# Optimization experiments

Hardware: AMD Instinct MI355X
Metric: run time of the kernel (lower is better)

Reference implementation:

```python
import jax, jax.numpy as jnp
import numpy as np

ATT_HEAD = 12
IN_DIM = 768
OUT_DIM = IN_DIM // ATT_HEAD
LEAKY_ALPHA = 0.2
B, N = 8, 512


def setup_inputs() -> dict:
    key = jax.random.key(0)
    ks = jax.random.split(key, 8)
    feat_in = jax.random.normal(ks[0], (B, N, IN_DIM), dtype=jnp.float32)
    adj = jax.random.randint(ks[1], (B, N, N), 0, 2) > 0
    # xavier_uniform for W: fan_in=in_dim, fan_out=out_dim
    lim_W = float(np.sqrt(6.0 / (IN_DIM + OUT_DIM)))
    W = jax.random.uniform(ks[2], (ATT_HEAD, IN_DIM, OUT_DIM), minval=-lim_W, maxval=lim_W, dtype=jnp.float32)
    b = jnp.zeros((OUT_DIM,), dtype=jnp.float32)
    lim_w = float(np.sqrt(6.0 / (OUT_DIM + 1)))
    w_src = jax.random.uniform(ks[3], (ATT_HEAD, OUT_DIM, 1), minval=-lim_w, maxval=lim_w, dtype=jnp.float32)
    w_dst = jax.random.uniform(ks[4], (ATT_HEAD, OUT_DIM, 1), minval=-lim_w, maxval=lim_w, dtype=jnp.float32)
    # xavier_normal for H.weight [in_dim, in_dim]
    std_H = float(np.sqrt(2.0 / (IN_DIM + IN_DIM)))
    H_w = jax.random.normal(ks[5], (IN_DIM, IN_DIM), dtype=jnp.float32) * std_H
    H_b = jax.random.normal(ks[6], (IN_DIM,), dtype=jnp.float32) * 0.01
    return {"feat_in": feat_in, "adj": adj, "W": W, "b": b,
            "w_src": w_src, "w_dst": w_dst, "H_w": H_w, "H_b": H_b}


def reference(feat_in, adj, W, b, w_src, w_dst, H_w, H_b):
    # h: [B, heads, N, out_dim]
    h = jnp.einsum('bnd,ade->bane', feat_in, W)
    th = jnp.tanh(h)
    attn_src = jnp.einsum('bane,aeo->bano', th, w_src)  # [B,A,N,1]
    attn_dst = jnp.einsum('bane,aeo->bano', th, w_dst)  # [B,A,N,1]
    attn = attn_src + jnp.swapaxes(attn_dst, 2, 3)      # [B,A,N,N]
    attn = jnp.where(attn >= 0, attn, LEAKY_ALPHA * attn)
    mask = ~adj[:, None, :, :]                           # [B,1,N,N]
    attn = jnp.where(mask, jnp.float32(-999.0), attn)
    attn = jax.nn.softmax(attn, axis=-1)
    feat_out = jnp.einsum('banm,bame->bane', attn, h) + b
    feat_out = jnp.swapaxes(feat_out, 1, 2).reshape(feat_in.shape[0], feat_in.shape[1], -1)
    feat_out = jax.nn.elu(feat_out)
    gate = jax.nn.sigmoid(feat_in @ H_w.T + H_b)
    return gate * feat_out + (1.0 - gate) * feat_in
```

## Files before the change

kernel.cpp:

```cpp
#include <hip/hip_runtime.h>
#include <hip/hip_bf16.h>

#define BB 8
#define NN 512
#define AH 12
#define DIN 768
#define EE 64
#define MM (BB*NN)
#define YY (BB*AH)
#define LEAKY 0.2f

typedef unsigned short u16;
typedef unsigned int u32;
typedef __attribute__((ext_vector_type(8))) short short8;
typedef __attribute__((ext_vector_type(4))) float f32x4;
typedef __attribute__((ext_vector_type(4))) u32 u32x4;

static __device__ __forceinline__ u16 f2bf(float f) {
    u32 u = __builtin_bit_cast(u32, f);
    u32 r = (u + 0x7FFFu + ((u >> 16) & 1u)) >> 16;
    return (u16)r;
}
static __device__ __forceinline__ u32 pk2(float a, float b) {
    return (u32)f2bf(a) | ((u32)f2bf(b) << 16);
}
static __device__ __forceinline__ u32 pk2t(float a, float b) {
    return (__builtin_bit_cast(u32, a) >> 16) | (__builtin_bit_cast(u32, b) & 0xFFFF0000u);
}
static __device__ __forceinline__ float ftanh(float x) {
    x = fminf(fmaxf(x, -15.f), 15.f);
    return 1.f - 2.f / (__expf(2.f * x) + 1.f);
}
static __device__ __forceinline__ void gl_lds16(const u16* g, u16* l) {
    __builtin_amdgcn_global_load_lds((const __attribute__((address_space(1))) unsigned int*)g,
                                     (__attribute__((address_space(3))) unsigned int*)l,
                                     16, 0, 0);
}

static __device__ __forceinline__ void mfma_probe(int lane, int* prow, int* pcol) {
    int q = lane >> 4, x = lane & 15;
    short8 af, bf;
#pragma unroll
    for (int j = 0; j < 8; j++) {
        int k = q * 8 + j;
        af[j] = (short)f2bf((k < 16) ? (float)(x * 16 + k) : 0.f);
        bf[j] = (short)f2bf((k == x) ? 1.f : 0.f);
    }
    f32x4 d = {};
    d = __builtin_amdgcn_mfma_f32_16x16x32_bf16(af, bf, d, 0, 0, 0);
#pragma unroll
    for (int r = 0; r < 4; r++) {
        int v = (int)(d[r] + 0.5f);
        prow[r] = v >> 4;
        pcol[r] = v & 15;
    }
}

#define N_FEAT (MM*DIN)
#define N_W    (AH*DIN*EE)
#define PACK_BLOCKS (MM/4)
#define CONV_BLOCKS ((N_FEAT + 2*N_W)/256)
__global__ __launch_bounds__(256) void prep_kernel(const int* __restrict__ adj,
                                                   const float* __restrict__ feat,
                                                   const float* __restrict__ W,
                                                   const float* __restrict__ Hw,
                                                   u32* __restrict__ maskbuf,
                                                   u16* __restrict__ featb,
                                                   u16* __restrict__ Wt,
                                                   u16* __restrict__ Hwb) {
    int blk = blockIdx.x, t = threadIdx.x;
    if (blk < PACK_BLOCKS) {
        int w = t >> 6, ln = t & 63;
        int row = blk * 4 + w;
        const int* ar = adj + (size_t)row * NN;
#pragma unroll
        for (int it = 0; it < 8; it++) {
            unsigned long long bal = __ballot(ar[it * 64 + ln] != 0);
            if (ln == 0) {
                maskbuf[row * 16 + it * 2]     = (u32)bal;
                maskbuf[row * 16 + it * 2 + 1] = (u32)(bal >> 32);
            }
        }
        return;
    }
    int i = (blk - PACK_BLOCKS) * 256 + t;
    if (i < N_FEAT) { featb[i] = f2bf(feat[i]); return; }
    int i2 = i - N_FEAT;
    if (i2 < N_W) {
        int a = i2 / (DIN * EE), rem = i2 % (DIN * EE);
        int e = rem / DIN, d = rem % DIN;
        Wt[i2] = f2bf(W[a * (DIN * EE) + d * EE + e]);
        return;
    }
    int i3 = i2 - N_W;
    Hwb[i3] = f2bf(Hw[i3]);
}

#define GEMM_CORE(Abase, Bbase)                                               \
    int wm = w & 1, wn = w >> 1, xr = x & 7;                                  \
    int srow = t >> 3;                                                        \
    int skoff = ((t & 7) ^ (srow & 7)) * 8;                                   \
    const u16* Agp = (Abase) + srow * DIN + skoff;                            \
    const u16* Bgp = (Bbase) + srow * DIN + skoff;                            \
    u16* Asw = As + w * 512;                                                  \
    u16* Bsw = Bs + w * 512;                                                  \
    const u16* ApA = As + (wm * 32 + x) * 64;                                 \
    const u16* ApB = Bs + (wn * 32 + x) * 64;                                 \
    f32x4 acc00 = {}, acc01 = {}, acc10 = {}, acc11 = {};                     \
    for (int k0 = 0; k0 < DIN; k0 += 64) {                                    \
        gl_lds16(Agp + k0, Asw);                                              \
        gl_lds16(Agp + 32 * DIN + k0, Asw + 2048);                            \
        gl_lds16(Bgp + k0, Bsw);                                              \
        gl_lds16(Bgp + 32 * DIN + k0, Bsw + 2048);                            \
        __syncthreads();                                                      \
        _Pragma("unroll")                                                     \
        for (int kk = 0; kk < 2; kk++) {                                      \
            int c8 = ((q + kk * 4) ^ xr) * 8;                                 \
            short8 a0 = *(const short8*)(ApA + c8);                           \
            short8 a1 = *(const short8*)(ApA + 16 * 64 + c8);                 \
            short8 b0 = *(const short8*)(ApB + c8);                           \
            short8 b1 = *(const short8*)(ApB + 16 * 64 + c8);                 \
            acc00 = __builtin_amdgcn_mfma_f32_16x16x32_bf16(a0, b0, acc00, 0, 0, 0); \
            acc01 = __builtin_amdgcn_mfma_f32_16x16x32_bf16(a0, b1, acc01, 0, 0, 0); \
            acc10 = __builtin_amdgcn_mfma_f32_16x16x32_bf16(a1, b0, acc10, 0, 0, 0); \
            acc11 = __builtin_amdgcn_mfma_f32_16x16x32_bf16(a1, b1, acc11, 0, 0, 0); \
        }                                                                     \
        __syncthreads();                                                      \
    }                                                                         \
    int prow[4], pcol[4];                                                     \
    mfma_probe(lane, prow, pcol);                                             \
    _Pragma("unroll")                                                         \
    for (int r = 0; r < 4; r++) {                                             \
        cs[wm * 32 + prow[r]][wn * 32 + pcol[r]]           = acc00[r];        \
        cs[wm * 32 + prow[r]][wn * 32 + 16 + pcol[r]]      = acc01[r];        \
        cs[wm * 32 + 16 + prow[r]][wn * 32 + pcol[r]]      = acc10[r];        \
        cs[wm * 32 + 16 + prow[r]][wn * 32 + 16 + pcol[r]] = acc11[r];        \
    }                                                                         \
    __syncthreads();

static __device__ __forceinline__ float sigm(float z) {
    z = fminf(fmaxf(z, -80.f), 80.f);
    return 1.f / (1.f + __expf(-z));
}

__global__ __launch_bounds__(256) void gemm_fused_kernel(const u16* __restrict__ featb,
                                                         const u16* __restrict__ Wt,
                                                         const u16* __restrict__ Hwb,
                                                         const float* __restrict__ wsrc,
                                                         const float* __restrict__ wdst,
                                                         const float* __restrict__ Hb,
                                                         u16* __restrict__ hT,
                                                         float2* __restrict__ Spair,
                                                         float2* __restrict__ Dpair,
                                                         float* __restrict__ Gbuf) {
    __shared__ u16 As[64 * 64];
    __shared__ u16 Bs[64 * 64];
    __shared__ alignas(16) float cs[64][68];
    int t = threadIdx.x, w = t >> 6, lane = t & 63, q = lane >> 4, x = lane & 15;
    int m0 = blockIdx.x * 64;
    int yb = blockIdx.y;

    if (yb < AH) {
        int a = yb;
        GEMM_CORE(featb + (size_t)m0 * DIN, Wt + (size_t)a * EE * DIN)

        int b = m0 >> 9;
        int y = b * AH + a;
        int nbase = m0 & 511;
        {
            int e = t >> 2, ng = t & 3;
            u32* dst = (u32*)&hT[((size_t)y * EE + e) * NN + nbase + ng * 16];
#pragma unroll
            for (int i = 0; i < 8; i++)
                dst[i] = pk2(cs[ng * 16 + 2 * i][e], cs[ng * 16 + 2 * i + 1][e]);
        }
        {
            int r = t >> 2, cg = t & 3;
            float s = 0.f, d = 0.f;
#pragma unroll
            for (int i = 0; i < 16; i++) {
                int e2 = cg * 16 + i;
                float th = ftanh(cs[r][e2]);
                s += th * wsrc[a * EE + e2];
                d += th * wdst[a * EE + e2];
            }
            s += __shfl_xor(s, 1); s += __shfl_xor(s, 2);
            d += __shfl_xor(d, 1); d += __shfl_xor(d, 2);
            if (cg == 0) {
                s = fminf(fmaxf(s, -40.f), 40.f);
                d = fminf(fmaxf(d, -40.f), 40.f);
                Spair[y * NN + nbase + r] = make_float2(__expf(s), __expf(0.2f * s));
                Dpair[y * NN + nbase + r] = make_float2(__expf(d), __expf(0.2f * d));
            }
        }
    } else {
        int n0 = (yb - AH) * 64;
        GEMM_CORE(featb + (size_t)m0 * DIN, Hwb + (size_t)n0 * DIN)

        float4 hb = *(const float4*)&Hb[n0 + (t & 15) * 4];
#pragma unroll
        for (int p = 0; p < 4; p++) {
            int ml = p * 16 + (t >> 4), c4 = (t & 15) * 4;
            float4 v4 = *(const float4*)&cs[ml][c4];
            size_t idx = (size_t)(m0 + ml) * DIN + n0 + c4;
            float4 o;
            o.x = sigm(v4.x + hb.x);
            o.y = sigm(v4.y + hb.y);
            o.z = sigm(v4.z + hb.z);
            o.w = sigm(v4.w + hb.w);
            *(float4*)&Gbuf[idx] = o;
        }
    }
}

__global__ __launch_bounds__(256) void attn_kernel(const u16* __restrict__ hT,
                                                   const float2* __restrict__ Spair,
                                                   const float2* __restrict__ Dpair,
                                                   const u32* __restrict__ maskbuf,
                                                   const float* __restrict__ bias,
                                                   const float* __restrict__ Gbuf,
                                                   const float* __restrict__ feat,
                                                   float* __restrict__ out) {
    __shared__ alignas(16) float2 sd2[NN];
    __shared__ u32 smask[64][17];
    __shared__ float silv[64];
    __shared__ alignas(16) float cs[64][68];

    int t = threadIdx.x;
    int y = blockIdx.y, bb = y / AH, a = y % AH;
    int i0 = blockIdx.x * 64;

    sd2[t] = Dpair[y * NN + t];
    sd2[t + 256] = Dpair[y * NN + 256 + t];
#pragma unroll
    for (int p = 0; p < 4; p++) {
        int idx = p * 256 + t, r = idx >> 4, c = idx & 15;
        smask[r][c] = maskbuf[((bb << 9) + i0 + r) * 16 + c];
    }
    __syncthreads();

    int w = t >> 6, lane = t & 63, q = lane >> 4, x = lane & 15;
    int rowl = w * 16 + x;
    float2 se = Spair[y * NN + i0 + rowl];
    float es1 = se.x, es2 = se.y;

    u32 anym = 0;
#pragma unroll
    for (int c = 0; c < 16; c++) anym |= smask[rowl][c];
    int uni = (anym == 0);

    const u16* hTy = hT + (size_t)y * EE * NN;
    f32x4 acc[4] = {};
    float lsum = 0.f;

#pragma unroll 2
    for (int k0 = 0; k0 < NN; k0 += 32) {
        u32 mb = smask[rowl][k0 >> 5] >> (q * 8);
        float pv[8];
#pragma unroll
        for (int j = 0; j < 8; j++) {
            float2 dp = sd2[k0 + q * 8 + j];
            float m1 = es1 * dp.x;
            float m2 = es2 * dp.y;
            float p = (m1 >= 1.f) ? m1 : m2;
            p = ((mb >> j) & 1) ? p : 0.f;
            p = uni ? 1.0f : p;
            lsum += p;
            pv[j] = p;
        }
        short8 af = __builtin_bit_cast(short8, (u32x4){
            pk2t(pv[0], pv[1]), pk2t(pv[2], pv[3]),
            pk2t(pv[4], pv[5]), pk2t(pv[6], pv[7])});
        const u16* hp = hTy + (size_t)x * NN + k0 + q * 8;
        short8 b0 = *(const short8*)(hp);
        short8 b1 = *(const short8*)(hp + 16 * NN);
        short8 b2 = *(const short8*)(hp + 32 * NN);
        short8 b3 = *(const short8*)(hp + 48 * NN);
        acc[0] = __builtin_amdgcn_mfma_f32_16x16x32_bf16(af, b0, acc[0], 0, 0, 0);
        acc[1] = __builtin_amdgcn_mfma_f32_16x16x32_bf16(af, b1, acc[1], 0, 0, 0);
        acc[2] = __builtin_amdgcn_mfma_f32_16x16x32_bf16(af, b2, acc[2], 0, 0, 0);
        acc[3] = __builtin_amdgcn_mfma_f32_16x16x32_bf16(af, b3, acc[3], 0, 0, 0);
    }

    lsum += __shfl_xor(lsum, 16);
    lsum += __shfl_xor(lsum, 32);
    if (q == 0) silv[rowl] = 1.f / fmaxf(lsum, 1e-30f);

    int prow[4], pcol[4];
    mfma_probe(lane, prow, pcol);
#pragma unroll
    for (int nt = 0; nt < 4; nt++)
#pragma unroll
        for (int r = 0; r < 4; r++)
            cs[w * 16 + prow[r]][nt * 16 + pcol[r]] = acc[nt][r];
    __syncthreads();

    float4 b4 = *(const float4*)&bias[(t & 15) * 4];
#pragma unroll
    for (int p = 0; p < 4; p++) {
        int nl = p * 16 + (t >> 4), e4 = (t & 15) * 4;
        float il = silv[nl];
        float4 c4 = *(const float4*)&cs[nl][e4];
        size_t base = ((size_t)(bb << 9) + i0 + nl) * DIN + a * EE + e4;
        float4 g4 = *(const float4*)&Gbuf[base];
        float4 f4 = *(const float4*)&feat[base];
        float4 o;
        float v, e;
        v = c4.x * il + b4.x; e = v > 0.f ? v : __expf(v) - 1.f; o.x = g4.x * e + (1.f - g4.x) * f4.x;
        v = c4.y * il + b4.y; e = v > 0.f ? v : __expf(v) - 1.f; o.y = g4.y * e + (1.f - g4.y) * f4.y;
        v = c4.z * il + b4.z; e = v > 0.f ? v : __expf(v) - 1.f; o.z = g4.z * e + (1.f - g4.z) * f4.z;
        v = c4.w * il + b4.w; e = v > 0.f ? v : __expf(v) - 1.f; o.w = g4.w * e + (1.f - g4.w) * f4.w;
        *(float4*)&out[base] = o;
    }
}

extern "C" void kernel_launch(void* const* d_in, const int* in_sizes, int n_in,
                              void* d_out, int out_size, void* d_ws, size_t ws_size,
                              hipStream_t stream) {
    const float* feat  = (const float*)d_in[0];
    const int*   adj   = (const int*)  d_in[1];
    const float* W     = (const float*)d_in[2];
    const float* bvec  = (const float*)d_in[3];
    const float* wsrc  = (const float*)d_in[4];
    const float* wdst  = (const float*)d_in[5];
    const float* Hw    = (const float*)d_in[6];
    const float* Hb    = (const float*)d_in[7];
    float* out = (float*)d_out;

    char* ws = (char*)d_ws;
    u16*    featb   = (u16*)(ws);
    u16*    Wt      = (u16*)(ws + 6291456);
    u16*    Hwb     = (u16*)(ws + 7471104);
    u16*    hT      = (u16*)(ws + 8650752);
    float2* Spair   = (float2*)(ws + 14942208);
    float2* Dpair   = (float2*)(ws + 15335424);
    u32*    maskbuf = (u32*)(ws + 15728640);
    float*  Gbuf    = (float*)(ws + 15990784);

    prep_kernel<<<PACK_BLOCKS + CONV_BLOCKS, 256, 0, stream>>>(
        adj, feat, W, Hw, maskbuf, featb, Wt, Hwb);
    gemm_fused_kernel<<<dim3(MM / 64, 2 * AH), 256, 0, stream>>>(
        featb, Wt, Hwb, wsrc, wdst, Hb, hT, Spair, Dpair, Gbuf);
    attn_kernel<<<dim3(NN / 64, YY), 256, 0, stream>>>(
        hT, Spair, Dpair, maskbuf, bvec, Gbuf, feat, out);
}
```

Before: 137.4 us.

## Move gate GEMM into attention kernel to eliminate Gbuf round trip

Moves the sigmoid gate GEMM (feat @ H_w^T) out of the first GEMM kernel and into the attention kernel. Each attention block now computes its own 64x64 gate tile in registers, with the GEMM staging buffers sharing LDS with the mask and Dpair arrays through a union. This removes the 12.6MB fp32 Gbuf write and read and halves the first GEMM's grid. In exchange, the attention kernel becomes longer and uses more registers, and the gate GEMM now runs serially before the attention work inside each block.

```diff
diff --git a/kernel.cpp b/kernel.cpp
--- a/kernel.cpp
+++ b/kernel.cpp
@@ -30,6 +30,10 @@
 static __device__ __forceinline__ float ftanh(float x) {
     x = fminf(fmaxf(x, -15.f), 15.f);
     return 1.f - 2.f / (__expf(2.f * x) + 1.f);
+}
+static __device__ __forceinline__ float sigm(float z) {
+    z = fminf(fmaxf(z, -80.f), 80.f);
+    return 1.f / (1.f + __expf(-z));
 }
 static __device__ __forceinline__ void gl_lds16(const u16* g, u16* l) {
     __builtin_amdgcn_global_load_lds((const __attribute__((address_space(1))) unsigned int*)g,
@@ -138,77 +142,48 @@
     }                                                                         \
     __syncthreads();
 
-static __device__ __forceinline__ float sigm(float z) {
-    z = fminf(fmaxf(z, -80.f), 80.f);
-    return 1.f / (1.f + __expf(-z));
-}
-
-__global__ __launch_bounds__(256) void gemm_fused_kernel(const u16* __restrict__ featb,
-                                                         const u16* __restrict__ Wt,
-                                                         const u16* __restrict__ Hwb,
-                                                         const float* __restrict__ wsrc,
-                                                         const float* __restrict__ wdst,
-                                                         const float* __restrict__ Hb,
-                                                         u16* __restrict__ hT,
-                                                         float2* __restrict__ Spair,
-                                                         float2* __restrict__ Dpair,
-                                                         float* __restrict__ Gbuf) {
+__global__ __launch_bounds__(256) void gemm_h_kernel(const u16* __restrict__ featb,
+                                                     const u16* __restrict__ Wt,
+                                                     const float* __restrict__ wsrc,
+                                                     const float* __restrict__ wdst,
+                                                     u16* __restrict__ hT,
+                                                     float2* __restrict__ Spair,
+                                                     float2* __restrict__ Dpair) {
     __shared__ u16 As[64 * 64];
     __shared__ u16 Bs[64 * 64];
     __shared__ alignas(16) float cs[64][68];
     int t = threadIdx.x, w = t >> 6, lane = t & 63, q = lane >> 4, x = lane & 15;
-    int m0 = blockIdx.x * 64;
-    int yb = blockIdx.y;
-
-    if (yb < AH) {
-        int a = yb;
-        GEMM_CORE(featb + (size_t)m0 * DIN, Wt + (size_t)a * EE * DIN)
-
-        int b = m0 >> 9;
-        int y = b * AH + a;
-        int nbase = m0 & 511;
-        {
-            int e = t >> 2, ng = t & 3;
-            u32* dst = (u32*)&hT[((size_t)y * EE + e) * NN + nbase + ng * 16];
-#pragma unroll
-            for (int i = 0; i < 8; i++)
-                dst[i] = pk2(cs[ng * 16 + 2 * i][e], cs[ng * 16 + 2 * i + 1][e]);
-        }
-        {
-            int r = t >> 2, cg = t & 3;
-            float s = 0.f, d = 0.f;
-#pragma unroll
-            for (int i = 0; i < 16; i++) {
-                int e2 = cg * 16 + i;
-                float th = ftanh(cs[r][e2]);
-                s += th * wsrc[a * EE + e2];
-                d += th * wdst[a * EE + e2];
-            }
-            s += __shfl_xor(s, 1); s += __shfl_xor(s, 2);
-            d += __shfl_xor(d, 1); d += __shfl_xor(d, 2);
-            if (cg == 0) {
-                s = fminf(fmaxf(s, -40.f), 40.f);
-                d = fminf(fmaxf(d, -40.f), 40.f);
-                Spair[y * NN + nbase + r] = make_float2(__expf(s), __expf(0.2f * s));
-                Dpair[y * NN + nbase + r] = make_float2(__expf(d), __expf(0.2f * d));
-            }
-        }
-    } else {
-        int n0 = (yb - AH) * 64;
-        GEMM_CORE(featb + (size_t)m0 * DIN, Hwb + (size_t)n0 * DIN)
-
-        float4 hb = *(const float4*)&Hb[n0 + (t & 15) * 4];
-#pragma unroll
-        for (int p = 0; p < 4; p++) {
-            int ml = p * 16 + (t >> 4), c4 = (t & 15) * 4;
-            float4 v4 = *(const float4*)&cs[ml][c4];
-            size_t idx = (size_t)(m0 + ml) * DIN + n0 + c4;
-            float4 o;
-            o.x = sigm(v4.x + hb.x);
-            o.y = sigm(v4.y + hb.y);
-            o.z = sigm(v4.z + hb.z);
-            o.w = sigm(v4.w + hb.w);
-            *(float4*)&Gbuf[idx] = o;
+    int m0 = blockIdx.x * 64, a = blockIdx.y;
+
+    GEMM_CORE(featb + (size_t)m0 * DIN, Wt + (size_t)a * EE * DIN)
+
+    int b = m0 >> 9;
+    int y = b * AH + a;
+    int nbase = m0 & 511;
+    {
+        int e = t >> 2, ng = t & 3;
+        u32* dst = (u32*)&hT[((size_t)y * EE + e) * NN + nbase + ng * 16];
+#pragma unroll
+        for (int i = 0; i < 8; i++)
+            dst[i] = pk2(cs[ng * 16 + 2 * i][e], cs[ng * 16 + 2 * i + 1][e]);
+    }
+    {
+        int r = t >> 2, cg = t & 3;
+        float s = 0.f, d = 0.f;
+#pragma unroll
+        for (int i = 0; i < 16; i++) {
+            int e2 = cg * 16 + i;
+            float th = ftanh(cs[r][e2]);
+            s += th * wsrc[a * EE + e2];
+            d += th * wdst[a * EE + e2];
+        }
+        s += __shfl_xor(s, 1); s += __shfl_xor(s, 2);
+        d += __shfl_xor(d, 1); d += __shfl_xor(d, 2);
+        if (cg == 0) {
+            s = fminf(fmaxf(s, -40.f), 40.f);
+            d = fminf(fmaxf(d, -40.f), 40.f);
+            Spair[y * NN + nbase + r] = make_float2(__expf(s), __expf(0.2f * s));
+            Dpair[y * NN + nbase + r] = make_float2(__expf(d), __expf(0.2f * d));
         }
     }
 }
@@ -218,18 +193,45 @@
                                                    const float2* __restrict__ Dpair,
                                                    const u32* __restrict__ maskbuf,
                                                    const float* __restrict__ bias,
-                                                   const float* __restrict__ Gbuf,
+                                                   const u16* __restrict__ featb,
+                                                   const u16* __restrict__ Hwb,
+                                                   const float* __restrict__ Hb,
                                                    const float* __restrict__ feat,
                                                    float* __restrict__ out) {
-    __shared__ alignas(16) float2 sd2[NN];
-    __shared__ u32 smask[64][17];
+    __shared__ union {
+        u16 stage[2][64 * 64];
+        struct {
+            float2 sd2[NN];
+            u32 smask[64][17];
+        } pv;
+    } ushr;
+    __shared__ alignas(16) float cs[64][68];
     __shared__ float silv[64];
-    __shared__ alignas(16) float cs[64][68];
 
     int t = threadIdx.x;
     int y = blockIdx.y, bb = y / AH, a = y % AH;
     int i0 = blockIdx.x * 64;
-
+    int w = t >> 6, lane = t & 63, q = lane >> 4, x = lane & 15;
+
+    float4 g4[4];
+    {
+        u16* As = ushr.stage[0];
+        u16* Bs = ushr.stage[1];
+        GEMM_CORE(featb + ((size_t)(bb << 9) + i0) * DIN, Hwb + (size_t)(a * EE) * DIN)
+        float4 hb = *(const float4*)&Hb[a * EE + (t & 15) * 4];
+#pragma unroll
+        for (int p = 0; p < 4; p++) {
+            int ml = p * 16 + (t >> 4), c4 = (t & 15) * 4;
+            float4 v4 = *(const float4*)&cs[ml][c4];
+            g4[p].x = sigm(v4.x + hb.x);
+            g4[p].y = sigm(v4.y + hb.y);
+            g4[p].z = sigm(v4.z + hb.z);
+            g4[p].w = sigm(v4.w + hb.w);
+        }
+    }
+
+    float2* sd2 = ushr.pv.sd2;
+    u32 (*smask)[17] = ushr.pv.smask;
     sd2[t] = Dpair[y * NN + t];
     sd2[t + 256] = Dpair[y * NN + 256 + t];
 #pragma unroll
@@ -239,7 +241,6 @@
     }
     __syncthreads();
 
-    int w = t >> 6, lane = t & 63, q = lane >> 4, x = lane & 15;
     int rowl = w * 16 + x;
     float2 se = Spair[y * NN + i0 + rowl];
     float es1 = se.x, es2 = se.y;
@@ -302,14 +303,14 @@
         float il = silv[nl];
         float4 c4 = *(const float4*)&cs[nl][e4];
         size_t base = ((size_t)(bb << 9) + i0 + nl) * DIN + a * EE + e4;
-        float4 g4 = *(const float4*)&Gbuf[base];
         float4 f4 = *(const float4*)&feat[base];
+        float4 g = g4[p];
         float4 o;
         float v, e;
-        v = c4.x * il + b4.x; e = v > 0.f ? v : __expf(v) - 1.f; o.x = g4.x * e + (1.f - g4.x) * f4.x;
-        v = c4.y * il + b4.y; e = v > 0.f ? v : __expf(v) - 1.f; o.y = g4.y * e + (1.f - g4.y) * f4.y;
-        v = c4.z * il + b4.z; e = v > 0.f ? v : __expf(v) - 1.f; o.z = g4.z * e + (1.f - g4.z) * f4.z;
-        v = c4.w * il + b4.w; e = v > 0.f ? v : __expf(v) - 1.f; o.w = g4.w * e + (1.f - g4.w) * f4.w;
+        v = c4.x * il + b4.x; e = v > 0.f ? v : __expf(v) - 1.f; o.x = g.x * e + (1.f - g.x) * f4.x;
+        v = c4.y * il + b4.y; e = v > 0.f ? v : __expf(v) - 1.f; o.y = g.y * e + (1.f - g.y) * f4.y;
+        v = c4.z * il + b4.z; e = v > 0.f ? v : __expf(v) - 1.f; o.z = g.z * e + (1.f - g.z) * f4.z;
+        v = c4.w * il + b4.w; e = v > 0.f ? v : __expf(v) - 1.f; o.w = g.w * e + (1.f - g.w) * f4.w;
         *(float4*)&out[base] = o;
     }
 }
@@ -335,12 +336,11 @@
     float2* Spair   = (float2*)(ws + 14942208);
     float2* Dpair   = (float2*)(ws + 15335424);
     u32*    maskbuf = (u32*)(ws + 15728640);
-    float*  Gbuf    = (float*)(ws + 15990784);
 
     prep_kernel<<<PACK_BLOCKS + CONV_BLOCKS, 256, 0, stream>>>(
         adj, feat, W, Hw, maskbuf, featb, Wt, Hwb);
-    gemm_fused_kernel<<<dim3(MM / 64, 2 * AH), 256, 0, stream>>>(
-        featb, Wt, Hwb, wsrc, wdst, Hb, hT, Spair, Dpair, Gbuf);
+    gemm_h_kernel<<<dim3(MM / 64, AH), 256, 0, stream>>>(
+        featb, Wt, wsrc, wdst, hT, Spair, Dpair);
     attn_kernel<<<dim3(NN / 64, YY), 256, 0, stream>>>(
-        hT, Spair, Dpair, maskbuf, bvec, Gbuf, feat, out);
-}
+        hT, Spair, Dpair, maskbuf, bvec, featb, Hwb, Hb, feat, out);
+}
```

Result: no change. 136.1 us (-0.9%).

## Merge W and gate GEMM blocks sharing feature tile; block hT layout

Applied to the files above, without the earlier changes.

Each GEMM block now computes both the per-head projection and the matching 64-column slice of the gate GEMM, so the feature tile is loaded into LDS once for both. The grid's y dimension shrinks from 2*AH to AH. hT is also re-laid out in 8-element k-chunks so that the attention kernel's B-operand loads become contiguous 16-byte vectors across lanes rather than strided rows. In exchange each block uses more LDS and accumulator registers and there are half as many blocks, which can lower occupancy.

```diff
diff --git a/kernel.cpp b/kernel.cpp
--- a/kernel.cpp
+++ b/kernel.cpp
@@ -30,6 +30,10 @@
 static __device__ __forceinline__ float ftanh(float x) {
     x = fminf(fmaxf(x, -15.f), 15.f);
     return 1.f - 2.f / (__expf(2.f * x) + 1.f);
+}
+static __device__ __forceinline__ float sigm(float z) {
+    z = fminf(fmaxf(z, -80.f), 80.f);
+    return 1.f / (1.f + __expf(-z));
 }
 static __device__ __forceinline__ void gl_lds16(const u16* g, u16* l) {
     __builtin_amdgcn_global_load_lds((const __attribute__((address_space(1))) unsigned int*)g,
@@ -96,53 +100,6 @@
     Hwb[i3] = f2bf(Hw[i3]);
 }
 
-#define GEMM_CORE(Abase, Bbase)                                               \
-    int wm = w & 1, wn = w >> 1, xr = x & 7;                                  \
-    int srow = t >> 3;                                                        \
-    int skoff = ((t & 7) ^ (srow & 7)) * 8;                                   \
-    const u16* Agp = (Abase) + srow * DIN + skoff;                            \
-    const u16* Bgp = (Bbase) + srow * DIN + skoff;                            \
-    u16* Asw = As + w * 512;                                                  \
-    u16* Bsw = Bs + w * 512;                                                  \
-    const u16* ApA = As + (wm * 32 + x) * 64;                                 \
-    const u16* ApB = Bs + (wn * 32 + x) * 64;                                 \
-    f32x4 acc00 = {}, acc01 = {}, acc10 = {}, acc11 = {};                     \
-    for (int k0 = 0; k0 < DIN; k0 += 64) {                                    \
-        gl_lds16(Agp + k0, Asw);                                              \
-        gl_lds16(Agp + 32 * DIN + k0, Asw + 2048);                            \
-        gl_lds16(Bgp + k0, Bsw);                                              \
-        gl_lds16(Bgp + 32 * DIN + k0, Bsw + 2048);                            \
-        __syncthreads();                                                      \
-        _Pragma("unroll")                                                     \
-        for (int kk = 0; kk < 2; kk++) {                                      \
-            int c8 = ((q + kk * 4) ^ xr) * 8;                                 \
-            short8 a0 = *(const short8*)(ApA + c8);                           \
-            short8 a1 = *(const short8*)(ApA + 16 * 64 + c8);                 \
-            short8 b0 = *(const short8*)(ApB + c8);                           \
-            short8 b1 = *(const short8*)(ApB + 16 * 64 + c8);                 \
-            acc00 = __builtin_amdgcn_mfma_f32_16x16x32_bf16(a0, b0, acc00, 0, 0, 0); \
-            acc01 = __builtin_amdgcn_mfma_f32_16x16x32_bf16(a0, b1, acc01, 0, 0, 0); \
-            acc10 = __builtin_amdgcn_mfma_f32_16x16x32_bf16(a1, b0, acc10, 0, 0, 0); \
-            acc11 = __builtin_amdgcn_mfma_f32_16x16x32_bf16(a1, b1, acc11, 0, 0, 0); \
-        }                                                                     \
-        __syncthreads();                                                      \
-    }                                                                         \
-    int prow[4], pcol[4];                                                     \
-    mfma_probe(lane, prow, pcol);                                             \
-    _Pragma("unroll")                                                         \
-    for (int r = 0; r < 4; r++) {                                             \
-        cs[wm * 32 + prow[r]][wn * 32 + pcol[r]]           = acc00[r];        \
-        cs[wm * 32 + prow[r]][wn * 32 + 16 + pcol[r]]      = acc01[r];        \
-        cs[wm * 32 + 16 + prow[r]][wn * 32 + pcol[r]]      = acc10[r];        \
-        cs[wm * 32 + 16 + prow[r]][wn * 32 + 16 + pcol[r]] = acc11[r];        \
-    }                                                                         \
-    __syncthreads();
-
-static __device__ __forceinline__ float sigm(float z) {
-    z = fminf(fmaxf(z, -80.f), 80.f);
-    return 1.f / (1.f + __expf(-z));
-}
-
 __global__ __launch_bounds__(256) void gemm_fused_kernel(const u16* __restrict__ featb,
                                                          const u16* __restrict__ Wt,
                                                          const u16* __restrict__ Hwb,
@@ -154,49 +111,117 @@
                                                          float2* __restrict__ Dpair,
                                                          float* __restrict__ Gbuf) {
     __shared__ u16 As[64 * 64];
-    __shared__ u16 Bs[64 * 64];
+    __shared__ u16 BsW[64 * 64];
+    __shared__ u16 BsG[64 * 64];
     __shared__ alignas(16) float cs[64][68];
     int t = threadIdx.x, w = t >> 6, lane = t & 63, q = lane >> 4, x = lane & 15;
-    int m0 = blockIdx.x * 64;
-    int yb = blockIdx.y;
-
-    if (yb < AH) {
-        int a = yb;
-        GEMM_CORE(featb + (size_t)m0 * DIN, Wt + (size_t)a * EE * DIN)
-
-        int b = m0 >> 9;
-        int y = b * AH + a;
-        int nbase = m0 & 511;
-        {
-            int e = t >> 2, ng = t & 3;
-            u32* dst = (u32*)&hT[((size_t)y * EE + e) * NN + nbase + ng * 16];
-#pragma unroll
-            for (int i = 0; i < 8; i++)
-                dst[i] = pk2(cs[ng * 16 + 2 * i][e], cs[ng * 16 + 2 * i + 1][e]);
-        }
-        {
-            int r = t >> 2, cg = t & 3;
-            float s = 0.f, d = 0.f;
-#pragma unroll
-            for (int i = 0; i < 16; i++) {
-                int e2 = cg * 16 + i;
-                float th = ftanh(cs[r][e2]);
-                s += th * wsrc[a * EE + e2];
-                d += th * wdst[a * EE + e2];
-            }
-            s += __shfl_xor(s, 1); s += __shfl_xor(s, 2);
-            d += __shfl_xor(d, 1); d += __shfl_xor(d, 2);
-            if (cg == 0) {
-                s = fminf(fmaxf(s, -40.f), 40.f);
-                d = fminf(fmaxf(d, -40.f), 40.f);
-                Spair[y * NN + nbase + r] = make_float2(__expf(s), __expf(0.2f * s));
-                Dpair[y * NN + nbase + r] = make_float2(__expf(d), __expf(0.2f * d));
-            }
-        }
-    } else {
-        int n0 = (yb - AH) * 64;
-        GEMM_CORE(featb + (size_t)m0 * DIN, Hwb + (size_t)n0 * DIN)
-
+    int m0 = blockIdx.x * 64, a = blockIdx.y;
+
+    int wm = w & 1, wn = w >> 1, xr = x & 7;
+    int srow = t >> 3;
+    int skoff = ((t & 7) ^ (srow & 7)) * 8;
+    const u16* Agp  = featb + (size_t)m0 * DIN + srow * DIN + skoff;
+    const u16* BWgp = Wt + (size_t)a * EE * DIN + srow * DIN + skoff;
+    const u16* BGgp = Hwb + (size_t)(a * EE) * DIN + srow * DIN + skoff;
+    u16* Asw  = As  + w * 512;
+    u16* BWsw = BsW + w * 512;
+    u16* BGsw = BsG + w * 512;
+    const u16* ApA  = As  + (wm * 32 + x) * 64;
+    const u16* ApBW = BsW + (wn * 32 + x) * 64;
+    const u16* ApBG = BsG + (wn * 32 + x) * 64;
+    f32x4 aW00 = {}, aW01 = {}, aW10 = {}, aW11 = {};
+    f32x4 aG00 = {}, aG01 = {}, aG10 = {}, aG11 = {};
+
+    for (int k0 = 0; k0 < DIN; k0 += 64) {
+        gl_lds16(Agp + k0, Asw);
+        gl_lds16(Agp + 32 * DIN + k0, Asw + 2048);
+        gl_lds16(BWgp + k0, BWsw);
+        gl_lds16(BWgp + 32 * DIN + k0, BWsw + 2048);
+        gl_lds16(BGgp + k0, BGsw);
+        gl_lds16(BGgp + 32 * DIN + k0, BGsw + 2048);
+        __syncthreads();
+#pragma unroll
+        for (int kk = 0; kk < 2; kk++) {
+            int c8 = ((q + kk * 4) ^ xr) * 8;
+            short8 a0 = *(const short8*)(ApA + c8);
+            short8 a1 = *(const short8*)(ApA + 16 * 64 + c8);
+            short8 bW0 = *(const short8*)(ApBW + c8);
+            short8 bW1 = *(const short8*)(ApBW + 16 * 64 + c8);
+            short8 bG0 = *(const short8*)(ApBG + c8);
+            short8 bG1 = *(const short8*)(ApBG + 16 * 64 + c8);
+            aW00 = __builtin_amdgcn_mfma_f32_16x16x32_bf16(a0, bW0, aW00, 0, 0, 0);
+            aW01 = __builtin_amdgcn_mfma_f32_16x16x32_bf16(a0, bW1, aW01, 0, 0, 0);
+            aW10 = __builtin_amdgcn_mfma_f32_16x16x32_bf16(a1, bW0, aW10, 0, 0, 0);
+            aW11 = __builtin_amdgcn_mfma_f32_16x16x32_bf16(a1, bW1, aW11, 0, 0, 0);
+            aG00 = __builtin_amdgcn_mfma_f32_16x16x32_bf16(a0, bG0, aG00, 0, 0, 0);
+            aG01 = __builtin_amdgcn_mfma_f32_16x16x32_bf16(a0, bG1, aG01, 0, 0, 0);
+            aG10 = __builtin_amdgcn_mfma_f32_16x16x32_bf16(a1, bG0, aG10, 0, 0, 0);
+            aG11 = __builtin_amdgcn_mfma_f32_16x16x32_bf16(a1, bG1, aG11, 0, 0, 0);
+        }
+        __syncthreads();
+    }
+
+    int prow[4], pcol[4];
+    mfma_probe(lane, prow, pcol);
+
+#pragma unroll
+    for (int r = 0; r < 4; r++) {
+        cs[wm * 32 + prow[r]][wn * 32 + pcol[r]]           = aW00[r];
+        cs[wm * 32 + prow[r]][wn * 32 + 16 + pcol[r]]      = aW01[r];
+        cs[wm * 32 + 16 + prow[r]][wn * 32 + pcol[r]]      = aW10[r];
+        cs[wm * 32 + 16 + prow[r]][wn * 32 + 16 + pcol[r]] = aW11[r];
+    }
+    __syncthreads();
+
+    int b = m0 >> 9;
+    int y = b * AH + a;
+    int nbase = m0 & 511;
+    {
+        int kcb = nbase >> 3;
+#pragma unroll
+        for (int i = 0; i < 2; i++) {
+            int idx = i * 256 + t;
+            int kcl = idx >> 6, e = idx & 63;
+            int r0 = kcl * 8;
+            u32x4 wv = { pk2(cs[r0 + 0][e], cs[r0 + 1][e]),
+                         pk2(cs[r0 + 2][e], cs[r0 + 3][e]),
+                         pk2(cs[r0 + 4][e], cs[r0 + 5][e]),
+                         pk2(cs[r0 + 6][e], cs[r0 + 7][e]) };
+            *(u32x4*)&hT[((((size_t)y << 6) + kcb + kcl) << 6 | e) * 8] = wv;
+        }
+    }
+    {
+        int r = t >> 2, cg = t & 3;
+        float s = 0.f, d = 0.f;
+#pragma unroll
+        for (int i = 0; i < 16; i++) {
+            int e2 = cg * 16 + i;
+            float th = ftanh(cs[r][e2]);
+            s += th * wsrc[a * EE + e2];
+            d += th * wdst[a * EE + e2];
+        }
+        s += __shfl_xor(s, 1); s += __shfl_xor(s, 2);
+        d += __shfl_xor(d, 1); d += __shfl_xor(d, 2);
+        if (cg == 0) {
+            s = fminf(fmaxf(s, -40.f), 40.f);
+            d = fminf(fmaxf(d, -40.f), 40.f);
+            Spair[y * NN + nbase + r] = make_float2(__expf(s), __expf(0.2f * s));
+            Dpair[y * NN + nbase + r] = make_float2(__expf(d), __expf(0.2f * d));
+        }
+    }
+    __syncthreads();
+
+#pragma unroll
+    for (int r = 0; r < 4; r++) {
+        cs[wm * 32 + prow[r]][wn * 32 + pcol[r]]           = aG00[r];
+        cs[wm * 32 + prow[r]][wn * 32 + 16 + pcol[r]]      = aG01[r];
+        cs[wm * 32 + 16 + prow[r]][wn * 32 + pcol[r]]      = aG10[r];
+        cs[wm * 32 + 16 + prow[r]][wn * 32 + 16 + pcol[r]] = aG11[r];
+    }
+    __syncthreads();
+
+    {
+        int n0 = a * EE;
         float4 hb = *(const float4*)&Hb[n0 + (t & 15) * 4];
 #pragma unroll
         for (int p = 0; p < 4; p++) {
@@ -229,6 +254,7 @@
     int t = threadIdx.x;
     int y = blockIdx.y, bb = y / AH, a = y % AH;
     int i0 = blockIdx.x * 64;
+    int w = t >> 6, lane = t & 63, q = lane >> 4, x = lane & 15;
 
     sd2[t] = Dpair[y * NN + t];
     sd2[t + 256] = Dpair[y * NN + 256 + t];
@@ -239,7 +265,6 @@
     }
     __syncthreads();
 
-    int w = t >> 6, lane = t & 63, q = lane >> 4, x = lane & 15;
     int rowl = w * 16 + x;
     float2 se = Spair[y * NN + i0 + rowl];
     float es1 = se.x, es2 = se.y;
@@ -249,7 +274,7 @@
     for (int c = 0; c < 16; c++) anym |= smask[rowl][c];
     int uni = (anym == 0);
 
-    const u16* hTy = hT + (size_t)y * EE * NN;
+    const u16* hTy = hT + ((size_t)y << 12) * 8;
     f32x4 acc[4] = {};
     float lsum = 0.f;
 
@@ -271,11 +296,11 @@
         short8 af = __builtin_bit_cast(short8, (u32x4){
             pk2t(pv[0], pv[1]), pk2t(pv[2], pv[3]),
             pk2t(pv[4], pv[5]), pk2t(pv[6], pv[7])});
-        const u16* hp = hTy + (size_t)x * NN + k0 + q * 8;
+        const u16* hp = hTy + ((((k0 >> 3) + q) << 6) + x) * 8;
         short8 b0 = *(const short8*)(hp);
-        short8 b1 = *(const short8*)(hp + 16 * NN);
-        short8 b2 = *(const short8*)(hp + 32 * NN);
-        short8 b3 = *(const short8*)(hp + 48 * NN);
+        short8 b1 = *(const short8*)(hp + 16 * 8);
+        short8 b2 = *(const short8*)(hp + 32 * 8);
+        short8 b3 = *(const short8*)(hp + 48 * 8);
         acc[0] = __builtin_amdgcn_mfma_f32_16x16x32_bf16(af, b0, acc[0], 0, 0, 0);
         acc[1] = __builtin_amdgcn_mfma_f32_16x16x32_bf16(af, b1, acc[1], 0, 0, 0);
         acc[2] = __builtin_amdgcn_mfma_f32_16x16x32_bf16(af, b2, acc[2], 0, 0, 0);
@@ -339,7 +364,7 @@
 
     prep_kernel<<<PACK_BLOCKS + CONV_BLOCKS, 256, 0, stream>>>(
         adj, feat, W, Hw, maskbuf, featb, Wt, Hwb);
-    gemm_fused_kernel<<<dim3(MM / 64, 2 * AH), 256, 0, stream>>>(
+    gemm_fused_kernel<<<dim3(MM / 64, AH), 256, 0, stream>>>(
         featb, Wt, Hwb, wsrc, wdst, Hb, hT, Spair, Dpair, Gbuf);
     attn_kernel<<<dim3(NN / 64, YY), 256, 0, stream>>>(
         hT, Spair, Dpair, maskbuf, bvec, Gbuf, feat, out);
```

After: 122.8 us. 10.6% less time.
